# Performance work log

Hardware: AMD Instinct MI355X
Metric: run time of the kernel (lower is better)

The kernel has to match this reference:

```python
import jax, jax.numpy as jnp
import numpy as np

NEG_SLOPE = 0.01  # nn.LeakyReLU default

N = 100000
E = 1600000
D_IN = 128
D_OUT = 128


def setup_inputs() -> dict:
    key = jax.random.key(0)
    ks = jax.random.split(key, 8)
    features = jax.random.normal(ks[0], (N, D_IN), dtype=jnp.float32)
    adj_rows = jax.random.randint(ks[1], (E,), 0, N, dtype=jnp.int64)
    adj_cols = jax.random.randint(ks[2], (E,), 0, N, dtype=jnp.int64)
    adj_vals = jax.random.uniform(ks[3], (E,), dtype=jnp.float32)
    s1 = 1.0 / np.sqrt(D_IN)
    W1 = jax.random.uniform(ks[4], (D_IN, D_OUT), jnp.float32, -s1, s1)
    b1 = jax.random.uniform(ks[5], (D_OUT,), jnp.float32, -s1, s1)
    W2 = jax.random.uniform(ks[6], (D_IN, D_OUT), jnp.float32, -s1, s1)
    b2 = jax.random.uniform(ks[7], (D_OUT,), jnp.float32, -s1, s1)
    return {"features": features, "adj_rows": adj_rows, "adj_cols": adj_cols,
            "adj_vals": adj_vals, "W1": W1, "b1": b1, "W2": W2, "b2": b2}


def reference(features, adj_rows, adj_cols, adj_vals, W1, b1, W2, b2):
    # h_neigh = adj @ features  (COO SpMM via gather + segment_sum)
    msgs = adj_vals[:, None] * features[adj_cols]          # [E, D_IN]
    h_neigh = jax.ops.segment_sum(msgs, adj_rows, num_segments=features.shape[0])
    term1 = (features + h_neigh) @ W1 + b1                 # W1(features + h_neigh)
    term2 = (features * h_neigh) @ W2 + b2                 # W2(features * h_neigh)
    pre = term1 + term2
    return jnp.where(pre >= 0, pre, NEG_SLOPE * pre)       # leaky_relu
```

## Files before the change

kernel.cpp:

```cpp
#include <hip/hip_runtime.h>

#define D 128
#define BM 64

typedef short short8 __attribute__((ext_vector_type(8)));
typedef unsigned short ushort8_t __attribute__((ext_vector_type(8)));
typedef float f32x4 __attribute__((ext_vector_type(4)));

__device__ __forceinline__ unsigned short f2bf(float x) {
    unsigned u = __float_as_uint(x);
    unsigned r = (u + 0x7fffu + ((u >> 16) & 1u)) >> 16;
    return (unsigned short)r;
}
__device__ __forceinline__ float bf2f(unsigned short u) {
    return __uint_as_float(((unsigned)u) << 16);
}

__global__ __launch_bounds__(256) void fconv_kernel(
    const float4* __restrict__ feat4, ushort4* __restrict__ fbf4, int total)
{
    int i = blockIdx.x * 256 + threadIdx.x;
    if (i < total) {
        float4 v = feat4[i];
        fbf4[i] = make_ushort4(f2bf(v.x), f2bf(v.y), f2bf(v.z), f2bf(v.w));
    }
}

__global__ __launch_bounds__(256) void wconv_kernel(
    const float* __restrict__ W1, const float* __restrict__ W2,
    unsigned short* __restrict__ WT)
{
    int idx = blockIdx.x * 256 + threadIdx.x;
    int c = idx & 127;
    int k = idx >> 7;
    float w = (k < 128) ? W1[k * 128 + c] : W2[(k - 128) * 128 + c];
    WT[c * 256 + k] = f2bf(w);
}


__global__ __launch_bounds__(256) void bucket_hist_kernel(
    const int* __restrict__ rows, int* __restrict__ bcnt, int E, int nb, int epb)
{
    __shared__ int cnt[1024];
    int t = threadIdx.x;
    for (int i = t; i < nb; i += 256) cnt[i] = 0;
    __syncthreads();
    int e0 = blockIdx.x * epb;
    int e1 = e0 + epb; if (e1 > E) e1 = E;
    for (int e = e0 + t; e < e1; e += 256) atomicAdd(&cnt[rows[e] >> 7], 1);
    __syncthreads();
    for (int i = t; i < nb; i += 256)
        if (cnt[i]) atomicAdd(&bcnt[i], cnt[i]);
}

__global__ __launch_bounds__(1024) void bucket_scan_kernel(
    const int* __restrict__ bcnt, int* __restrict__ bstart,
    int* __restrict__ bcur, int nb, int E)
{
    __shared__ int wsum[16];
    int tid = threadIdx.x, lane = tid & 63, wid = tid >> 6;
    int x = (tid < nb) ? bcnt[tid] : 0;
    int v = x;
    #pragma unroll
    for (int off = 1; off < 64; off <<= 1) {
        int y = __shfl_up(v, off, 64);
        if (lane >= off) v += y;
    }
    if (lane == 63) wsum[wid] = v;
    __syncthreads();
    if (wid == 0 && lane < 16) {
        int s = wsum[lane];
        #pragma unroll
        for (int off = 1; off < 16; off <<= 1) {
            int y = __shfl_up(s, off, 64);
            if (lane >= off) s += y;
        }
        wsum[lane] = s;
    }
    __syncthreads();
    int wexcl = wid ? wsum[wid - 1] : 0;
    int excl = wexcl + v - x;
    if (tid < nb) { bstart[tid] = excl; bcur[tid] = excl; }
    if (tid == 0) bstart[nb] = E;
}

__global__ __launch_bounds__(256) void bucket_scatter_kernel(
    const int* __restrict__ rows, const int* __restrict__ cols,
    const float* __restrict__ vals, int* __restrict__ bcur,
    uint2* __restrict__ bsedge, int E, int nb)
{
    __shared__ int cnt[1024];
    __shared__ int base[1024];
    int t = threadIdx.x;
    int e0 = blockIdx.x * 4096;
    for (int i = t; i < nb; i += 256) cnt[i] = 0;
    __syncthreads();
    #pragma unroll
    for (int q = 0; q < 16; ++q) {
        int e = e0 + t + q * 256;
        if (e < E) atomicAdd(&cnt[rows[e] >> 7], 1);
    }
    __syncthreads();
    for (int i = t; i < nb; i += 256) {
        int c = cnt[i];
        if (c) { base[i] = atomicAdd(&bcur[i], c); cnt[i] = 0; }
    }
    __syncthreads();
    #pragma unroll
    for (int q = 0; q < 16; ++q) {
        int e = e0 + t + q * 256;
        if (e < E) {
            int r = rows[e];
            int b = r >> 7;
            int pos = base[b] + atomicAdd(&cnt[b], 1);
            bsedge[pos] = make_uint2(((unsigned)(r & 127) << 17) | (unsigned)cols[e],
                                     __float_as_uint(vals[e]));
        }
    }
}

__global__ __launch_bounds__(256) void bucket_sort_kernel(
    const uint2* __restrict__ bsedge,
    const int* __restrict__ bstart,
    uint2* __restrict__ sedge,
    int* __restrict__ row_start,
    int N, int E)
{
    __shared__ int cnt[128];
    __shared__ int base[128];
    const int b = blockIdx.x;
    const int t = threadIdx.x;
    const int s = bstart[b], e = bstart[b + 1];
    if (t < 128) cnt[t] = 0;
    __syncthreads();
    for (int j = s + t; j < e; j += 256)
        atomicAdd(&cnt[bsedge[j].x >> 17], 1);
    __syncthreads();
    if (t < 64) {
        int c0 = cnt[2 * t], c1 = cnt[2 * t + 1];
        int pair = c0 + c1;
        int v = pair;
        #pragma unroll
        for (int off = 1; off < 64; off <<= 1) {
            int y = __shfl_up(v, off, 64);
            if (t >= off) v += y;
        }
        int excl = v - pair;
        base[2 * t]     = excl;
        base[2 * t + 1] = excl + c0;
        cnt[2 * t] = 0;
        cnt[2 * t + 1] = 0;
    }
    __syncthreads();
    const int r0 = b << 7;
    if (t < 128 && r0 + t < N) row_start[r0 + t] = s + base[t];
    if (b == 0 && t == 0) row_start[N] = E;
    for (int j = s + t; j < e; j += 256) {
        uint2 ed = bsedge[j];
        int rl = ed.x >> 17;
        int p = atomicAdd(&cnt[rl], 1);
        sedge[s + base[rl] + p] = make_uint2(ed.x & 0x1FFFFu, ed.y);
    }
}

__global__ __launch_bounds__(256) void spmm_gemm_kernel(
    const float4* __restrict__ feat4,
    const ushort8_t* __restrict__ fbf8,
    const int* __restrict__ row_start,
    const uint2* __restrict__ sedge,
    const unsigned short* __restrict__ WT,
    const float* __restrict__ b1, const float* __restrict__ b2,
    float* __restrict__ out, int N)
{
    __shared__ __align__(16) unsigned char am_raw[64 * 512];

    const int tid = threadIdx.x;
    const int block0 = blockIdx.x * BM;
    const int rq = tid >> 4;
    const int l  = tid & 15;

    for (int it = 0; it < 4; ++it) {
        int node = it * 16 + rq;
        int row = block0 + node;
        float acc[8] = {};
        float f[8] = {};
        if (row < N) {
            int s = row_start[row];
            int e = row_start[row + 1];
            int j = s;
            for (; j + 3 < e; j += 4) {
                uint2 e0 = sedge[j],     e1 = sedge[j + 1];
                uint2 e2 = sedge[j + 2], e3 = sedge[j + 3];
                ushort8_t f0 = fbf8[(size_t)e0.x * 16 + l];
                ushort8_t f1 = fbf8[(size_t)e1.x * 16 + l];
                ushort8_t f2 = fbf8[(size_t)e2.x * 16 + l];
                ushort8_t f3 = fbf8[(size_t)e3.x * 16 + l];
                float v0 = __uint_as_float(e0.y), v1 = __uint_as_float(e1.y);
                float v2 = __uint_as_float(e2.y), v3 = __uint_as_float(e3.y);
                #pragma unroll
                for (int q = 0; q < 8; ++q) {
                    acc[q] = fmaf(v0, bf2f(f0[q]), acc[q]);
                    acc[q] = fmaf(v1, bf2f(f1[q]), acc[q]);
                    acc[q] = fmaf(v2, bf2f(f2[q]), acc[q]);
                    acc[q] = fmaf(v3, bf2f(f3[q]), acc[q]);
                }
            }
            for (; j < e; ++j) {
                uint2 e0 = sedge[j];
                float v = __uint_as_float(e0.y);
                ushort8_t f0 = fbf8[(size_t)e0.x * 16 + l];
                #pragma unroll
                for (int q = 0; q < 8; ++q) acc[q] = fmaf(v, bf2f(f0[q]), acc[q]);
            }
            float4 fa = feat4[(size_t)row * 32 + 2 * l];
            float4 fb = feat4[(size_t)row * 32 + 2 * l + 1];
            f[0] = fa.x; f[1] = fa.y; f[2] = fa.z; f[3] = fa.w;
            f[4] = fb.x; f[5] = fb.y; f[6] = fb.z; f[7] = fb.w;
        }
        ushort8_t av, mv;
        #pragma unroll
        for (int q = 0; q < 8; ++q) {
            av[q] = f2bf(f[q] + acc[q]);
            mv[q] = f2bf(f[q] * acc[q]);
        }
        int swz = (node & 7) << 4;
        unsigned char* rowp = am_raw + node * 512;
        *(ushort8_t*)(rowp + ((16 * l) ^ swz))       = av;
        *(ushort8_t*)(rowp + 256 + ((16 * l) ^ swz)) = mv;
    }
    __syncthreads();

    const int lane = tid & 63;
    const int w    = tid >> 6;
    const int wr   = w >> 1;
    const int wc   = w & 1;
    const int l15  = lane & 15;
    const int lk   = lane >> 4;
    const int rswz = (l15 & 7) << 4;

    f32x4 gacc[2][4] = {};

    const char* WTc = (const char*)WT;
    const unsigned char* arow0 = am_raw + (wr * 32 + l15) * 512;
    const unsigned char* arow1 = arow0 + 16 * 512;

    #pragma unroll
    for (int ks = 0; ks < 8; ++ks) {
        int kbyte = ks * 64 + lk * 16;
        int akoff = kbyte ^ rswz;
        short8 a0 = *(const short8*)(arow0 + akoff);
        short8 a1 = *(const short8*)(arow1 + akoff);
        short8 bfr[4];
        #pragma unroll
        for (int nc = 0; nc < 4; ++nc) {
            int col = wc * 64 + nc * 16 + l15;
            bfr[nc] = *(const short8*)(WTc + col * 512 + kbyte);
        }
        #pragma unroll
        for (int nc = 0; nc < 4; ++nc) {
            gacc[0][nc] = __builtin_amdgcn_mfma_f32_16x16x32_bf16(a0, bfr[nc], gacc[0][nc], 0, 0, 0);
            gacc[1][nc] = __builtin_amdgcn_mfma_f32_16x16x32_bf16(a1, bfr[nc], gacc[1][nc], 0, 0, 0);
        }
    }

    #pragma unroll
    for (int nc = 0; nc < 4; ++nc) {
        int col = wc * 64 + nc * 16 + l15;
        float bias = b1[col] + b2[col];
        #pragma unroll
        for (int mr = 0; mr < 2; ++mr) {
            int rbase = block0 + wr * 32 + mr * 16 + lk * 4;
            #pragma unroll
            for (int r = 0; r < 4; ++r) {
                int row = rbase + r;
                if (row < N) {
                    float v = gacc[mr][nc][r] + bias;
                    out[row * 128 + col] = (v >= 0.f) ? v : 0.01f * v;
                }
            }
        }
    }
}

__global__ __launch_bounds__(256) void spmm_ab_kernel(
    const float4* __restrict__ feat4,
    const ushort8_t* __restrict__ fbf8,
    const int* __restrict__ row_start,
    const uint2* __restrict__ sedge,
    unsigned char* __restrict__ ambf, int N)
{
    int t = blockIdx.x * 256 + threadIdx.x;
    int row = t >> 4;
    int l   = t & 15;
    if (row >= N) return;

    int s = row_start[row];
    int e = row_start[row + 1];

    float acc[8] = {};
    int j = s;
    for (; j + 1 < e; j += 2) {
        uint2 e0 = sedge[j], e1 = sedge[j + 1];
        float v0 = __uint_as_float(e0.y), v1 = __uint_as_float(e1.y);
        ushort8_t f0 = fbf8[(size_t)e0.x * 16 + l];
        ushort8_t f1 = fbf8[(size_t)e1.x * 16 + l];
        #pragma unroll
        for (int q = 0; q < 8; ++q) {
            acc[q] = fmaf(v0, bf2f(f0[q]), acc[q]);
            acc[q] = fmaf(v1, bf2f(f1[q]), acc[q]);
        }
    }
    if (j < e) {
        uint2 e0 = sedge[j];
        float v = __uint_as_float(e0.y);
        ushort8_t f = fbf8[(size_t)e0.x * 16 + l];
        #pragma unroll
        for (int q = 0; q < 8; ++q) acc[q] = fmaf(v, bf2f(f[q]), acc[q]);
    }

    float4 fa = feat4[(size_t)row * 32 + 2 * l];
    float4 fb = feat4[(size_t)row * 32 + 2 * l + 1];
    float f[8] = { fa.x, fa.y, fa.z, fa.w, fb.x, fb.y, fb.z, fb.w };

    ushort8_t av, mv;
    #pragma unroll
    for (int q = 0; q < 8; ++q) {
        av[q] = f2bf(f[q] + acc[q]);
        mv[q] = f2bf(f[q] * acc[q]);
    }

    int swz = (row & 7) << 4;
    unsigned char* rowp = ambf + (size_t)row * 512;
    *(ushort8_t*)(rowp + ((16 * l) ^ swz))       = av;
    *(ushort8_t*)(rowp + 256 + ((16 * l) ^ swz)) = mv;
}

__global__ __launch_bounds__(256) void mfma_gemm2_kernel(
    const unsigned char* __restrict__ ambf,
    const unsigned short* __restrict__ WT,
    const float* __restrict__ b1, const float* __restrict__ b2,
    float* __restrict__ out, int N)
{
    __shared__ __align__(16) unsigned char am_raw[64 * 512];

    const int tid = threadIdx.x;
    const int block0 = blockIdx.x * BM;

    const short8* src = (const short8*)(ambf + (size_t)block0 * 512);
    short8* dst = (short8*)am_raw;
    #pragma unroll
    for (int it = 0; it < 8; ++it) {
        int idx = tid + it * 256;
        dst[idx] = src[idx];
    }
    __syncthreads();

    const int lane = tid & 63;
    const int w    = tid >> 6;
    const int wr   = w >> 1;
    const int wc   = w & 1;
    const int l15  = lane & 15;
    const int lk   = lane >> 4;
    const int rswz = (l15 & 7) << 4;

    f32x4 acc[2][4] = {};

    const char* WTc = (const char*)WT;
    const unsigned char* arow0 = am_raw + (wr * 32 + l15) * 512;
    const unsigned char* arow1 = arow0 + 16 * 512;

    #pragma unroll
    for (int ks = 0; ks < 8; ++ks) {
        int kbyte = ks * 64 + lk * 16;
        int akoff = kbyte ^ rswz;
        short8 a0 = *(const short8*)(arow0 + akoff);
        short8 a1 = *(const short8*)(arow1 + akoff);
        short8 bfr[4];
        #pragma unroll
        for (int nc = 0; nc < 4; ++nc) {
            int col = wc * 64 + nc * 16 + l15;
            bfr[nc] = *(const short8*)(WTc + col * 512 + kbyte);
        }
        #pragma unroll
        for (int nc = 0; nc < 4; ++nc) {
            acc[0][nc] = __builtin_amdgcn_mfma_f32_16x16x32_bf16(a0, bfr[nc], acc[0][nc], 0, 0, 0);
            acc[1][nc] = __builtin_amdgcn_mfma_f32_16x16x32_bf16(a1, bfr[nc], acc[1][nc], 0, 0, 0);
        }
    }

    #pragma unroll
    for (int nc = 0; nc < 4; ++nc) {
        int col = wc * 64 + nc * 16 + l15;
        float bias = b1[col] + b2[col];
        #pragma unroll
        for (int mr = 0; mr < 2; ++mr) {
            int rbase = block0 + wr * 32 + mr * 16 + lk * 4;
            #pragma unroll
            for (int r = 0; r < 4; ++r) {
                int row = rbase + r;
                if (row < N) {
                    float v = acc[mr][nc][r] + bias;
                    out[row * 128 + col] = (v >= 0.f) ? v : 0.01f * v;
                }
            }
        }
    }
}

__global__ __launch_bounds__(256) void hist_kernel(
    const int* __restrict__ rows, int* __restrict__ counts, int E)
{
    int e = blockIdx.x * 256 + threadIdx.x;
    if (e < E) atomicAdd(&counts[rows[e]], 1);
}

__global__ __launch_bounds__(256) void scan_pass1(
    const int* __restrict__ counts, int* __restrict__ btot, int N)
{
    int tid = threadIdx.x;
    int i = blockIdx.x * 1024 + tid * 4;
    int s = 0;
    if (i + 3 < N) {
        int4 v = *(const int4*)(counts + i);
        s = v.x + v.y + v.z + v.w;
    } else {
        for (int q = 0; q < 4; ++q) if (i + q < N) s += counts[i + q];
    }
    #pragma unroll
    for (int off = 32; off >= 1; off >>= 1) s += __shfl_down(s, off, 64);
    __shared__ int ws[4];
    if ((tid & 63) == 0) ws[tid >> 6] = s;
    __syncthreads();
    if (tid == 0) btot[blockIdx.x] = ws[0] + ws[1] + ws[2] + ws[3];
}

__global__ __launch_bounds__(1024) void scan_pass2(
    const int* __restrict__ btot, int* __restrict__ boff, int nb)
{
    __shared__ int wsum[16];
    int tid = threadIdx.x, lane = tid & 63, wid = tid >> 6;
    int x = (tid < nb) ? btot[tid] : 0;
    int v = x;
    #pragma unroll
    for (int off = 1; off < 64; off <<= 1) {
        int y = __shfl_up(v, off, 64);
        if (lane >= off) v += y;
    }
    if (lane == 63) wsum[wid] = v;
    __syncthreads();
    if (wid == 0 && lane < 16) {
        int s = wsum[lane];
        #pragma unroll
        for (int off = 1; off < 16; off <<= 1) {
            int y = __shfl_up(s, off, 64);
            if (lane >= off) s += y;
        }
        wsum[lane] = s;
    }
    __syncthreads();
    int wexcl = wid ? wsum[wid - 1] : 0;
    if (tid < nb) boff[tid] = wexcl + v - x;
}

__global__ __launch_bounds__(256) void scan_pass3(
    int* __restrict__ row_start, int* __restrict__ cursor,
    const int* __restrict__ boff, int N, int E)
{
    int tid = threadIdx.x;
    int base = blockIdx.x * 1024 + tid * 4;
    int c0 = 0, c1 = 0, c2 = 0, c3 = 0;
    if (base + 3 < N) {
        int4 v = *(const int4*)(row_start + base);
        c0 = v.x; c1 = v.y; c2 = v.z; c3 = v.w;
    } else {
        if (base + 0 < N) c0 = row_start[base + 0];
        if (base + 1 < N) c1 = row_start[base + 1];
        if (base + 2 < N) c2 = row_start[base + 2];
        if (base + 3 < N) c3 = row_start[base + 3];
    }
    int s0 = c0, s1 = s0 + c1, s2 = s1 + c2, s3 = s2 + c3;
    int lane = tid & 63, wid = tid >> 6;
    int v = s3;
    #pragma unroll
    for (int off = 1; off < 64; off <<= 1) {
        int y = __shfl_up(v, off, 64);
        if (lane >= off) v += y;
    }
    __shared__ int ws[4];
    if (lane == 63) ws[wid] = v;
    __syncthreads();
    int wexcl = 0;
    for (int q = 0; q < wid; ++q) wexcl += ws[q];
    int texcl = wexcl + (v - s3) + boff[blockIdx.x];
    int e0 = texcl, e1 = texcl + s0, e2 = texcl + s1, e3 = texcl + s2;
    if (base + 0 < N) { row_start[base + 0] = e0; cursor[base + 0] = e0; }
    if (base + 1 < N) { row_start[base + 1] = e1; cursor[base + 1] = e1; }
    if (base + 2 < N) { row_start[base + 2] = e2; cursor[base + 2] = e2; }
    if (base + 3 < N) { row_start[base + 3] = e3; cursor[base + 3] = e3; }
    if (blockIdx.x == 0 && tid == 0) row_start[N] = E;
}

__global__ __launch_bounds__(256) void scatter_sort_kernel(
    const int* __restrict__ rows, const int* __restrict__ cols,
    const float* __restrict__ vals, int* __restrict__ cursor,
    uint2* __restrict__ sedge, int E)
{
    int e = blockIdx.x * 256 + threadIdx.x;
    if (e < E) {
        int r = rows[e];
        int p = atomicAdd(&cursor[r], 1);
        sedge[p] = make_uint2((unsigned)cols[e], __float_as_uint(vals[e]));
    }
}

__global__ __launch_bounds__(256) void spmm_kernel(
    const float2* __restrict__ feat2,
    const int* __restrict__ row_start,
    const uint2* __restrict__ sedge,
    float2* __restrict__ h2, int N)
{
    int gw = (blockIdx.x * 256 + threadIdx.x) >> 6;
    int lane = threadIdx.x & 63;
    if (gw >= N) return;
    int s = row_start[gw];
    int e = row_start[gw + 1];
    float2 acc = make_float2(0.f, 0.f);
    int j = s;
    for (; j + 1 < e; j += 2) {
        uint2 e0 = sedge[j], e1 = sedge[j + 1];
        float v0 = __uint_as_float(e0.y), v1 = __uint_as_float(e1.y);
        float2 f0 = feat2[(size_t)e0.x * 64 + lane];
        float2 f1 = feat2[(size_t)e1.x * 64 + lane];
        acc.x = fmaf(v0, f0.x, acc.x);
        acc.y = fmaf(v0, f0.y, acc.y);
        acc.x = fmaf(v1, f1.x, acc.x);
        acc.y = fmaf(v1, f1.y, acc.y);
    }
    if (j < e) {
        uint2 e0 = sedge[j];
        float v = __uint_as_float(e0.y);
        float2 f = feat2[(size_t)e0.x * 64 + lane];
        acc.x = fmaf(v, f.x, acc.x);
        acc.y = fmaf(v, f.y, acc.y);
    }
    h2[(size_t)gw * 64 + lane] = acc;
}

__global__ __launch_bounds__(256) void mfma_gemm_kernel(
    const float4* __restrict__ feat4, const float4* __restrict__ h4,
    const unsigned short* __restrict__ WT,
    const float* __restrict__ b1, const float* __restrict__ b2,
    float* __restrict__ out, int N)
{
    __shared__ __align__(16) unsigned char am_raw[64 * 512];
    const int tid = threadIdx.x;
    const int block0 = blockIdx.x * BM;
    #pragma unroll
    for (int it = 0; it < 8; ++it) {
        int idx  = tid + it * 256;
        int node = idx >> 5;
        int p    = idx & 31;
        int g    = block0 + node;
        float4 fv = make_float4(0.f, 0.f, 0.f, 0.f);
        float4 hv = make_float4(0.f, 0.f, 0.f, 0.f);
        if (g < N) { fv = feat4[g * 32 + p]; hv = h4[g * 32 + p]; }
        ushort4 av = make_ushort4(f2bf(fv.x + hv.x), f2bf(fv.y + hv.y),
                                  f2bf(fv.z + hv.z), f2bf(fv.w + hv.w));
        ushort4 mv = make_ushort4(f2bf(fv.x * hv.x), f2bf(fv.y * hv.y),
                                  f2bf(fv.z * hv.z), f2bf(fv.w * hv.w));
        int swz = (node & 7) << 4;
        *(ushort4*)(am_raw + node * 512 + ((p * 8) ^ swz))       = av;
        *(ushort4*)(am_raw + node * 512 + ((256 + p * 8) ^ swz)) = mv;
    }
    __syncthreads();
    const int lane = tid & 63;
    const int w    = tid >> 6;
    const int wr   = w >> 1;
    const int wc   = w & 1;
    const int l15  = lane & 15;
    const int lk   = lane >> 4;
    const int rswz = (l15 & 7) << 4;
    f32x4 acc[2][4] = {};
    const char* WTc = (const char*)WT;
    const unsigned char* arow0 = am_raw + (wr * 32 + l15) * 512;
    const unsigned char* arow1 = arow0 + 16 * 512;
    #pragma unroll
    for (int ks = 0; ks < 8; ++ks) {
        int kbyte = ks * 64 + lk * 16;
        int akoff = kbyte ^ rswz;
        short8 a0 = *(const short8*)(arow0 + akoff);
        short8 a1 = *(const short8*)(arow1 + akoff);
        short8 bfr[4];
        #pragma unroll
        for (int nc = 0; nc < 4; ++nc) {
            int col = wc * 64 + nc * 16 + l15;
            bfr[nc] = *(const short8*)(WTc + col * 512 + kbyte);
        }
        #pragma unroll
        for (int nc = 0; nc < 4; ++nc) {
            acc[0][nc] = __builtin_amdgcn_mfma_f32_16x16x32_bf16(a0, bfr[nc], acc[0][nc], 0, 0, 0);
            acc[1][nc] = __builtin_amdgcn_mfma_f32_16x16x32_bf16(a1, bfr[nc], acc[1][nc], 0, 0, 0);
        }
    }
    #pragma unroll
    for (int nc = 0; nc < 4; ++nc) {
        int col = wc * 64 + nc * 16 + l15;
        float bias = b1[col] + b2[col];
        #pragma unroll
        for (int mr = 0; mr < 2; ++mr) {
            int rbase = block0 + wr * 32 + mr * 16 + lk * 4;
            #pragma unroll
            for (int r = 0; r < 4; ++r) {
                int row = rbase + r;
                if (row < N) {
                    float v = acc[mr][nc][r] + bias;
                    out[row * 128 + col] = (v >= 0.f) ? v : 0.01f * v;
                }
            }
        }
    }
}

__global__ __launch_bounds__(256) void edge_scatter_kernel(
    const float4* __restrict__ feat4, const int* __restrict__ rows,
    const int* __restrict__ cols, const float* __restrict__ vals,
    float* __restrict__ h, int E)
{
    int idx = blockIdx.x * 256 + threadIdx.x;
    if (idx >= E * 32) return;
    int e = idx >> 5;
    int p = idx & 31;
    int r = rows[e];
    int c = cols[e];
    float v = vals[e];
    float4 f = feat4[c * 32 + p];
    float* hr = h + (long long)r * D + p * 4;
    unsafeAtomicAdd(hr + 0, v * f.x);
    unsafeAtomicAdd(hr + 1, v * f.y);
    unsafeAtomicAdd(hr + 2, v * f.z);
    unsafeAtomicAdd(hr + 3, v * f.w);
}

__global__ __launch_bounds__(256) void fused_gemm_kernel(
    const float* __restrict__ feat, const float* __restrict__ h,
    const float* __restrict__ W1, const float* __restrict__ b1,
    const float* __restrict__ W2, const float* __restrict__ b2,
    float* __restrict__ out, int N)
{
    __shared__ float a_lds[BM][D];
    __shared__ float m_lds[BM][D];
    const int tid = threadIdx.x;
    const int block0 = blockIdx.x * BM;
    const float4* feat4 = (const float4*)feat;
    const float4* h4    = (const float4*)h;
    #pragma unroll
    for (int it = 0; it < 8; ++it) {
        int idx  = tid + it * 256;
        int node = idx >> 5;
        int p    = idx & 31;
        int gnode = block0 + node;
        float4 fv = make_float4(0.f, 0.f, 0.f, 0.f);
        float4 hv = make_float4(0.f, 0.f, 0.f, 0.f);
        if (gnode < N) { fv = feat4[gnode * 32 + p]; hv = h4[gnode * 32 + p]; }
        float4 av = make_float4(fv.x + hv.x, fv.y + hv.y, fv.z + hv.z, fv.w + hv.w);
        float4 mv = make_float4(fv.x * hv.x, fv.y * hv.y, fv.z * hv.z, fv.w * hv.w);
        *(float4*)&a_lds[node][p * 4] = av;
        *(float4*)&m_lds[node][p * 4] = mv;
    }
    __syncthreads();
    const int c = tid & 31;
    const int g = tid >> 5;
    float acc[8][4] = {};
    const float4* W1v = (const float4*)W1;
    const float4* W2v = (const float4*)W2;
    for (int k = 0; k < D; ++k) {
        float4 w1 = W1v[k * 32 + c];
        float4 w2 = W2v[k * 32 + c];
        #pragma unroll
        for (int t = 0; t < 8; ++t) {
            float av = a_lds[g + 8 * t][k];
            float mv = m_lds[g + 8 * t][k];
            acc[t][0] = fmaf(av, w1.x, fmaf(mv, w2.x, acc[t][0]));
            acc[t][1] = fmaf(av, w1.y, fmaf(mv, w2.y, acc[t][1]));
            acc[t][2] = fmaf(av, w1.z, fmaf(mv, w2.z, acc[t][2]));
            acc[t][3] = fmaf(av, w1.w, fmaf(mv, w2.w, acc[t][3]));
        }
    }
    float4 bb1 = ((const float4*)b1)[c];
    float4 bb2 = ((const float4*)b2)[c];
    const float bx = bb1.x + bb2.x, by = bb1.y + bb2.y;
    const float bz = bb1.z + bb2.z, bw = bb1.w + bb2.w;
    #pragma unroll
    for (int t = 0; t < 8; ++t) {
        int gnode = block0 + g + 8 * t;
        if (gnode >= N) continue;
        float4 o;
        o.x = acc[t][0] + bx; o.y = acc[t][1] + by;
        o.z = acc[t][2] + bz; o.w = acc[t][3] + bw;
        o.x = (o.x >= 0.f) ? o.x : 0.01f * o.x;
        o.y = (o.y >= 0.f) ? o.y : 0.01f * o.y;
        o.z = (o.z >= 0.f) ? o.z : 0.01f * o.z;
        o.w = (o.w >= 0.f) ? o.w : 0.01f * o.w;
        ((float4*)out)[gnode * 32 + c] = o;
    }
}

extern "C" void kernel_launch(void* const* d_in, const int* in_sizes, int n_in,
                              void* d_out, int out_size, void* d_ws, size_t ws_size,
                              hipStream_t stream) {
    const float* feat = (const float*)d_in[0];
    const int*   rows = (const int*)d_in[1];
    const int*   cols = (const int*)d_in[2];
    const float* vals = (const float*)d_in[3];
    const float* W1   = (const float*)d_in[4];
    const float* b1   = (const float*)d_in[5];
    const float* W2   = (const float*)d_in[6];
    const float* b2   = (const float*)d_in[7];

    const int N = in_sizes[0] / D;
    const int E = in_sizes[1];
    float* out = (float*)d_out;

    const int NBK  = (N + 127) >> 7;
    const int Npad = NBK << 7;

    size_t off = 0;
    unsigned short* featbf = (unsigned short*)d_ws;                off += (size_t)N * D * 2;
    off = (off + 15) & ~(size_t)15;
    uint2* sedge = (uint2*)((char*)d_ws + off);                    off += (size_t)E * 8;
    unsigned short* WT = (unsigned short*)((char*)d_ws + off);     off += 128 * 256 * 2;
    int* row_start = (int*)((char*)d_ws + off);                    off += (size_t)(N + 1) * 4;
    off = (off + 15) & ~(size_t)15;
    uint2* bsedge = (uint2*)((char*)d_ws + off);                   off += (size_t)E * 8;
    int* bcnt   = (int*)((char*)d_ws + off);                       off += (size_t)NBK * 4;
    int* bstart = (int*)((char*)d_ws + off);                       off += (size_t)(NBK + 1) * 4;
    int* bcur   = (int*)((char*)d_ws + off);                       off += (size_t)NBK * 4;
    size_t need1a = off;

    if (ws_size >= need1a && NBK <= 1024 && N <= (1 << 17)) {
        hipMemsetAsync(bcnt, 0, (size_t)NBK * sizeof(int), stream);
        fconv_kernel<<<(N * 32 + 255) / 256, 256, 0, stream>>>(
            (const float4*)feat, (ushort4*)featbf, N * 32);
        wconv_kernel<<<128, 256, 0, stream>>>(W1, W2, WT);
        int epb = (E + 255) / 256;
        bucket_hist_kernel<<<256, 256, 0, stream>>>(rows, bcnt, E, NBK, epb);
        bucket_scan_kernel<<<1, 1024, 0, stream>>>(bcnt, bstart, bcur, NBK, E);
        bucket_scatter_kernel<<<(E + 4095) / 4096, 256, 0, stream>>>(
            rows, cols, vals, bcur, bsedge, E, NBK);
        bucket_sort_kernel<<<NBK, 256, 0, stream>>>(
            bsedge, bstart, sedge, row_start, N, E);
        spmm_gemm_kernel<<<(N + BM - 1) / BM, 256, 0, stream>>>(
            (const float4*)feat, (const ushort8_t*)featbf, row_start, sedge,
            WT, b1, b2, out, N);
        return;
    }

    const int NB = (N + 1023) / 1024;
    off = 0;
    unsigned char* ambf = (unsigned char*)d_ws;                    off += (size_t)Npad * 512;
    featbf = (unsigned short*)((char*)d_ws + off);                 off += (size_t)N * D * 2;
    off = (off + 15) & ~(size_t)15;
    sedge = (uint2*)((char*)d_ws + off);                           off += (size_t)E * 8;
    WT = (unsigned short*)((char*)d_ws + off);                     off += 128 * 256 * 2;
    row_start = (int*)((char*)d_ws + off);                         off += (size_t)(N + 1) * 4;
    off = (off + 15) & ~(size_t)15;
    int* cursor = (int*)((char*)d_ws + off);                       off += (size_t)N * 4;
    int* btot = (int*)((char*)d_ws + off);                         off += (size_t)NB * 4;
    int* boff = (int*)((char*)d_ws + off);                         off += (size_t)NB * 4;
    size_t need1b = off;

    if (ws_size >= need1b && NB <= 1024) {
        hipMemsetAsync(row_start, 0, (size_t)(N + 1) * sizeof(int), stream);
        fconv_kernel<<<(N * 32 + 255) / 256, 256, 0, stream>>>(
            (const float4*)feat, (ushort4*)featbf, N * 32);
        wconv_kernel<<<128, 256, 0, stream>>>(W1, W2, WT);
        hist_kernel<<<(E + 255) / 256, 256, 0, stream>>>(rows, row_start, E);
        scan_pass1<<<NB, 256, 0, stream>>>(row_start, btot, N);
        scan_pass2<<<1, 1024, 0, stream>>>(btot, boff, NB);
        scan_pass3<<<NB, 256, 0, stream>>>(row_start, cursor, boff, N, E);
        scatter_sort_kernel<<<(E + 255) / 256, 256, 0, stream>>>(
            rows, cols, vals, cursor, sedge, E);
        spmm_ab_kernel<<<(N * 16 + 255) / 256, 256, 0, stream>>>(
            (const float4*)feat, (const ushort8_t*)featbf, row_start, sedge,
            ambf, N);
        mfma_gemm2_kernel<<<(N + BM - 1) / BM, 256, 0, stream>>>(
            ambf, WT, b1, b2, out, N);
        return;
    }

    off = 0;
    float* h = (float*)d_ws;                           off += (size_t)N * D * 4;
    int* row_start2 = (int*)((char*)d_ws + off);       off += (size_t)(N + 1) * 4;
    int* cursor2    = (int*)((char*)d_ws + off);       off += (size_t)N * 4;
    off = (off + 15) & ~(size_t)15;
    uint2* sedge2   = (uint2*)((char*)d_ws + off);     off += (size_t)E * 8;
    off = (off + 15) & ~(size_t)15;
    unsigned short* WT2 = (unsigned short*)((char*)d_ws + off); off += 128 * 256 * 2;
    int* btot2 = (int*)((char*)d_ws + off);            off += (size_t)NB * 4;
    int* boff2 = (int*)((char*)d_ws + off);            off += (size_t)NB * 4;
    size_t need2 = off;

    if (ws_size >= need2 && NB <= 1024) {
        hipMemsetAsync(row_start2, 0, (size_t)(N + 1) * sizeof(int), stream);
        wconv_kernel<<<128, 256, 0, stream>>>(W1, W2, WT2);
        hist_kernel<<<(E + 255) / 256, 256, 0, stream>>>(rows, row_start2, E);
        scan_pass1<<<NB, 256, 0, stream>>>(row_start2, btot2, N);
        scan_pass2<<<1, 1024, 0, stream>>>(btot2, boff2, NB);
        scan_pass3<<<NB, 256, 0, stream>>>(row_start2, cursor2, boff2, N, E);
        scatter_sort_kernel<<<(E + 255) / 256, 256, 0, stream>>>(
            rows, cols, vals, cursor2, sedge2, E);
        spmm_kernel<<<(N * 64 + 255) / 256, 256, 0, stream>>>(
            (const float2*)feat, row_start2, sedge2, (float2*)h, N);
        mfma_gemm_kernel<<<(N + BM - 1) / BM, 256, 0, stream>>>(
            (const float4*)feat, (const float4*)h, WT2, b1, b2, out, N);
        return;
    }

    size_t hbytes = (size_t)N * D * sizeof(float);
    float* hh = (ws_size >= hbytes) ? (float*)d_ws : out;
    hipMemsetAsync(hh, 0, hbytes, stream);
    edge_scatter_kernel<<<((size_t)E * 32 + 255) / 256, 256, 0, stream>>>(
        (const float4*)feat, rows, cols, vals, hh, E);
    fused_gemm_kernel<<<(N + BM - 1) / BM, 256, 0, stream>>>(
        feat, hh, W1, b1, W2, b2, out, N);
}
```

Measured before the change: 191.8 us.

## Shrink fused SpMM+GEMM block to 16 rows for more parallelism

The fused gather-SpMM + MFMA GEMM kernel now handles 16 rows per block instead of 64, with each thread doing a single row gather instead of looping over four. Each wave computes a 16x32 output slice in the GEMM phase. This raises block count and occupancy (smaller LDS footprint) and exposes more memory-level parallelism in the irregular gather. The trade-off is that each block reloads the full W^T from cache with less reuse per load.

```diff
diff --git a/kernel.cpp b/kernel.cpp
--- a/kernel.cpp
+++ b/kernel.cpp
@@ -163,7 +163,7 @@
     }
 }
 
-__global__ __launch_bounds__(256) void spmm_gemm_kernel(
+__global__ __launch_bounds__(256) void spmm_gemm16_kernel(
     const float4* __restrict__ feat4,
     const ushort8_t* __restrict__ fbf8,
     const int* __restrict__ row_start,
@@ -172,59 +172,58 @@
     const float* __restrict__ b1, const float* __restrict__ b2,
     float* __restrict__ out, int N)
 {
-    __shared__ __align__(16) unsigned char am_raw[64 * 512];
+    __shared__ __align__(16) unsigned char am_raw[16 * 512];
 
     const int tid = threadIdx.x;
-    const int block0 = blockIdx.x * BM;
+    const int block0 = blockIdx.x * 16;
     const int rq = tid >> 4;
     const int l  = tid & 15;
 
-    for (int it = 0; it < 4; ++it) {
-        int node = it * 16 + rq;
-        int row = block0 + node;
-        float acc[8] = {};
-        float f[8] = {};
-        if (row < N) {
-            int s = row_start[row];
-            int e = row_start[row + 1];
-            int j = s;
-            for (; j + 3 < e; j += 4) {
-                uint2 e0 = sedge[j],     e1 = sedge[j + 1];
-                uint2 e2 = sedge[j + 2], e3 = sedge[j + 3];
-                ushort8_t f0 = fbf8[(size_t)e0.x * 16 + l];
-                ushort8_t f1 = fbf8[(size_t)e1.x * 16 + l];
-                ushort8_t f2 = fbf8[(size_t)e2.x * 16 + l];
-                ushort8_t f3 = fbf8[(size_t)e3.x * 16 + l];
-                float v0 = __uint_as_float(e0.y), v1 = __uint_as_float(e1.y);
-                float v2 = __uint_as_float(e2.y), v3 = __uint_as_float(e3.y);
-                #pragma unroll
-                for (int q = 0; q < 8; ++q) {
-                    acc[q] = fmaf(v0, bf2f(f0[q]), acc[q]);
-                    acc[q] = fmaf(v1, bf2f(f1[q]), acc[q]);
-                    acc[q] = fmaf(v2, bf2f(f2[q]), acc[q]);
-                    acc[q] = fmaf(v3, bf2f(f3[q]), acc[q]);
-                }
+    int row = block0 + rq;
+    float acc[8] = {};
+    float f[8] = {};
+    if (row < N) {
+        int s = row_start[row];
+        int e = row_start[row + 1];
+        int j = s;
+        for (; j + 3 < e; j += 4) {
+            uint2 e0 = sedge[j],     e1 = sedge[j + 1];
+            uint2 e2 = sedge[j + 2], e3 = sedge[j + 3];
+            ushort8_t f0 = fbf8[(size_t)e0.x * 16 + l];
+            ushort8_t f1 = fbf8[(size_t)e1.x * 16 + l];
+            ushort8_t f2 = fbf8[(size_t)e2.x * 16 + l];
+            ushort8_t f3 = fbf8[(size_t)e3.x * 16 + l];
+            float v0 = __uint_as_float(e0.y), v1 = __uint_as_float(e1.y);
+            float v2 = __uint_as_float(e2.y), v3 = __uint_as_float(e3.y);
+            #pragma unroll
+            for (int q = 0; q < 8; ++q) {
+                acc[q] = fmaf(v0, bf2f(f0[q]), acc[q]);
+                acc[q] = fmaf(v1, bf2f(f1[q]), acc[q]);
+                acc[q] = fmaf(v2, bf2f(f2[q]), acc[q]);
+                acc[q] = fmaf(v3, bf2f(f3[q]), acc[q]);
             }
-            for (; j < e; ++j) {
-                uint2 e0 = sedge[j];
-                float v = __uint_as_float(e0.y);
-                ushort8_t f0 = fbf8[(size_t)e0.x * 16 + l];
-                #pragma unroll
-                for (int q = 0; q < 8; ++q) acc[q] = fmaf(v, bf2f(f0[q]), acc[q]);
-            }
-            float4 fa = feat4[(size_t)row * 32 + 2 * l];
-            float4 fb = feat4[(size_t)row * 32 + 2 * l + 1];
-            f[0] = fa.x; f[1] = fa.y; f[2] = fa.z; f[3] = fa.w;
-            f[4] = fb.x; f[5] = fb.y; f[6] = fb.z; f[7] = fb.w;
-        }
-        ushort8_t av, mv;
-        #pragma unroll
-        for (int q = 0; q < 8; ++q) {
-            av[q] = f2bf(f[q] + acc[q]);
-            mv[q] = f2bf(f[q] * acc[q]);
-        }
-        int swz = (node & 7) << 4;
-        unsigned char* rowp = am_raw + node * 512;
+        }
+        for (; j < e; ++j) {
+            uint2 e0 = sedge[j];
+            float v = __uint_as_float(e0.y);
+            ushort8_t f0 = fbf8[(size_t)e0.x * 16 + l];
+            #pragma unroll
+            for (int q = 0; q < 8; ++q) acc[q] = fmaf(v, bf2f(f0[q]), acc[q]);
+        }
+        float4 fa = feat4[(size_t)row * 32 + 2 * l];
+        float4 fb = feat4[(size_t)row * 32 + 2 * l + 1];
+        f[0] = fa.x; f[1] = fa.y; f[2] = fa.z; f[3] = fa.w;
+        f[4] = fb.x; f[5] = fb.y; f[6] = fb.z; f[7] = fb.w;
+    }
+    ushort8_t av, mv;
+    #pragma unroll
+    for (int q = 0; q < 8; ++q) {
+        av[q] = f2bf(f[q] + acc[q]);
+        mv[q] = f2bf(f[q] * acc[q]);
+    }
+    {
+        int swz = (rq & 7) << 4;
+        unsigned char* rowp = am_raw + rq * 512;
         *(ushort8_t*)(rowp + ((16 * l) ^ swz))       = av;
         *(ushort8_t*)(rowp + 256 + ((16 * l) ^ swz)) = mv;
     }
@@ -232,51 +231,37 @@
 
     const int lane = tid & 63;
     const int w    = tid >> 6;
-    const int wr   = w >> 1;
-    const int wc   = w & 1;
     const int l15  = lane & 15;
     const int lk   = lane >> 4;
     const int rswz = (l15 & 7) << 4;
 
-    f32x4 gacc[2][4] = {};
-
+    f32x4 gacc[2] = {};
     const char* WTc = (const char*)WT;
-    const unsigned char* arow0 = am_raw + (wr * 32 + l15) * 512;
-    const unsigned char* arow1 = arow0 + 16 * 512;
+    const unsigned char* arow = am_raw + l15 * 512;
 
     #pragma unroll
     for (int ks = 0; ks < 8; ++ks) {
         int kbyte = ks * 64 + lk * 16;
-        int akoff = kbyte ^ rswz;
-        short8 a0 = *(const short8*)(arow0 + akoff);
-        short8 a1 = *(const short8*)(arow1 + akoff);
-        short8 bfr[4];
-        #pragma unroll
-        for (int nc = 0; nc < 4; ++nc) {
-            int col = wc * 64 + nc * 16 + l15;
-            bfr[nc] = *(const short8*)(WTc + col * 512 + kbyte);
-        }
-        #pragma unroll
-        for (int nc = 0; nc < 4; ++nc) {
-            gacc[0][nc] = __builtin_amdgcn_mfma_f32_16x16x32_bf16(a0, bfr[nc], gacc[0][nc], 0, 0, 0);
-            gacc[1][nc] = __builtin_amdgcn_mfma_f32_16x16x32_bf16(a1, bfr[nc], gacc[1][nc], 0, 0, 0);
-        }
-    }
-
-    #pragma unroll
-    for (int nc = 0; nc < 4; ++nc) {
-        int col = wc * 64 + nc * 16 + l15;
+        short8 a = *(const short8*)(arow + (kbyte ^ rswz));
+        #pragma unroll
+        for (int nc = 0; nc < 2; ++nc) {
+            int col = w * 32 + nc * 16 + l15;
+            short8 b = *(const short8*)(WTc + col * 512 + kbyte);
+            gacc[nc] = __builtin_amdgcn_mfma_f32_16x16x32_bf16(a, b, gacc[nc], 0, 0, 0);
+        }
+    }
+
+    #pragma unroll
+    for (int nc = 0; nc < 2; ++nc) {
+        int col = w * 32 + nc * 16 + l15;
         float bias = b1[col] + b2[col];
-        #pragma unroll
-        for (int mr = 0; mr < 2; ++mr) {
-            int rbase = block0 + wr * 32 + mr * 16 + lk * 4;
-            #pragma unroll
-            for (int r = 0; r < 4; ++r) {
-                int row = rbase + r;
-                if (row < N) {
-                    float v = gacc[mr][nc][r] + bias;
-                    out[row * 128 + col] = (v >= 0.f) ? v : 0.01f * v;
-                }
+        int rbase = block0 + lk * 4;
+        #pragma unroll
+        for (int r = 0; r < 4; ++r) {
+            int orow = rbase + r;
+            if (orow < N) {
+                float v = gacc[nc][r] + bias;
+                out[orow * 128 + col] = (v >= 0.f) ? v : 0.01f * v;
             }
         }
     }
@@ -749,7 +734,7 @@
             rows, cols, vals, bcur, bsedge, E, NBK);
         bucket_sort_kernel<<<NBK, 256, 0, stream>>>(
             bsedge, bstart, sedge, row_start, N, E);
-        spmm_gemm_kernel<<<(N + BM - 1) / BM, 256, 0, stream>>>(
+        spmm_gemm16_kernel<<<(N + 15) / 16, 256, 0, stream>>>(
             (const float4*)feat, (const ushort8_t*)featbf, row_start, sedge,
             WT, b1, b2, out, N);
         return;
```

Measured after the change: 184.6 us. -3.8%, faster.
